# Kernel optimization log

Hardware: AMD Instinct MI355X
Metric: run time of the kernel (lower is better)

Reference implementation:

```python
import jax, jax.numpy as jnp
import numpy as np

# Static config matching init_kwargs
LA = 20.0
GAMMA_INV = 1.0 / 0.1   # self.gamma = 1/gamma
TAU = 0.2
MARGIN = 0.01 * 1.0      # margin * margin_scale
CN = 2
K = 2048
DIM = 128
SUMK = CN * K
B = 16384

# Static intra-class upper-triangular pair mask (same as self.weight in torch)
_blk = np.triu(np.ones((K, K), dtype=bool), k=1)
PAIR_MASK = np.zeros((SUMK, SUMK), dtype=bool)
for _i in range(CN):
    PAIR_MASK[_i * K:(_i + 1) * K, _i * K:(_i + 1) * K] = _blk
PAIR_MASK = jnp.asarray(PAIR_MASK)
N_PAIRS = float(CN * K * (K - 1) // 2)


def setup_inputs() -> dict:
    key = jax.random.key(0)
    k1, k2, k3 = jax.random.split(key, 3)
    x = jax.random.normal(k1, (B, DIM), dtype=jnp.float32)
    target = jax.random.randint(k2, (B,), 0, CN, dtype=jnp.int64)
    fc = jax.random.normal(k3, (DIM, SUMK), dtype=jnp.float32) * 0.05
    return {"x": x, "target": target, "fc": fc}


def reference(x, target, fc):
    # L2-normalize inputs (dim=1) and centers (dim=0)
    norm_input = x / jnp.linalg.norm(x, axis=1, keepdims=True)          # [B, DIM]
    centers = fc / jnp.linalg.norm(fc, axis=0, keepdims=True)           # [DIM, SUMK]

    simInd = norm_input @ centers                                       # [B, SUMK]
    sim = simInd.reshape(B, CN, K)                                      # per-class groups

    # softmax-weighted intra-class similarity (intra_max='softmax')
    prob = jax.nn.softmax(sim * GAMMA_INV, axis=-1)
    simClass = jnp.sum(prob * sim, axis=-1)                             # [B, CN]

    # NOTE: original code sets margin on ALL columns, so uniform shift
    logits = LA * (simClass - MARGIN)

    # cross-entropy, mean reduction (class weights are all 1)
    logp = jax.nn.log_softmax(logits, axis=-1)
    ce = -jnp.take_along_axis(logp, target[:, None].astype(jnp.int32), axis=1).mean()

    # center-pair regularizer (tau > 0, K > 1)
    simCenter = centers.T @ centers                                     # [SUMK, SUMK]
    d = jnp.sqrt(2.0 + 1e-5 - 2.0 * simCenter)                          # >=0 everywhere
    reg = jnp.sum(jnp.where(PAIR_MASK, d, 0.0)) / (N_PAIRS * 2.0)

    loss = ce + TAU * reg
    return loss, logits
```

## Files before the change

### kernel.cpp

```cpp
#include <hip/hip_runtime.h>
#include <math.h>

#define NB 16384
#define DIM 128
#define SUMK 4096
#define KCLS 2048

constexpr float LA = 20.0f;
constexpr float TAU = 0.2f;
constexpr float MARGIN = 0.01f;
constexpr float NPAIRS2 = 8384512.0f;
constexpr float G2L = 14.426950408889634f;
#define CS (8 * NB)

typedef _Float16 half8 __attribute__((ext_vector_type(8)));
typedef float f32x4 __attribute__((ext_vector_type(4)));

#if __has_builtin(__builtin_amdgcn_exp2f)
#define EXP2(v) __builtin_amdgcn_exp2f(v)
#else
#define EXP2(v) exp2f(v)
#endif

#define GLOAD_LDS(SRC, DST)                                                          \
    __builtin_amdgcn_global_load_lds(                                                \
        (const __attribute__((address_space(1))) void*)(SRC),                        \
        (__attribute__((address_space(3))) void*)(DST), 16, 0, 0)

__global__ __launch_bounds__(256) void knorm(const float* __restrict__ fc,
                                             _Float16* __restrict__ cnT) {
    const int t = threadIdx.x;
    const int lane = t & 63;
    const int wid = t >> 6;
    const int c = lane & 15;
    const int q = lane >> 4;
    const int j = blockIdx.x * 64 + wid * 16 + c;

    float v[32];
    const float* p = fc + (size_t)(q * 32) * SUMK + j;
    float ss = 0.f;
#pragma unroll
    for (int i = 0; i < 32; ++i) {
        v[i] = p[(size_t)i * SUMK];
        ss = fmaf(v[i], v[i], ss);
    }
    ss += __shfl_xor(ss, 16);
    ss += __shfl_xor(ss, 32);
    float rn = 1.0f / sqrtf(ss);

    _Float16* w = cnT + (size_t)j * DIM + q * 32;
#pragma unroll
    for (int s = 0; s < 4; ++s) {
        half8 h;
#pragma unroll
        for (int k = 0; k < 8; ++k) h[k] = (_Float16)(v[s * 8 + k] * rn);
        *(half8*)(w + s * 8) = h;
    }
}

__global__ __launch_bounds__(256, 4) void kbig(const float* __restrict__ x,
                                               const _Float16* __restrict__ cnT,
                                               float* __restrict__ pw,
                                               float* __restrict__ reg_acc) {
    __shared__ _Float16 smem[3][2][4][64][8];
    __shared__ float red[4];

    const int t = threadIdx.x;
    const int lane = t & 63;
    const int wid = t >> 6;
    const int m = lane & 15;
    const int kg = lane >> 4;
    const int id = blockIdx.x;

    if (id >= 1024) {
        const int rid = id - 1024;
        const int cls = rid >> 10;
        const int ti = (rid >> 5) & 31;
        const int tj = rid & 31;
        if (tj < ti) return;

        const int i0 = cls * KCLS + ti * 64 + wid * 16;
        const int jb = cls * KCLS + tj * 64;

        const _Float16* aip = cnT + (size_t)(i0 + m) * DIM + kg * 8;
        half8 af[4];
#pragma unroll
        for (int tt = 0; tt < 4; ++tt) af[tt] = *(const half8*)(aip + tt * 32);

        half8 bf[16];
#pragma unroll
        for (int fj = 0; fj < 4; ++fj) {
            const _Float16* bjp = cnT + (size_t)(jb + fj * 16 + m) * DIM + kg * 8;
#pragma unroll
            for (int tt = 0; tt < 4; ++tt) bf[fj * 4 + tt] = *(const half8*)(bjp + tt * 32);
        }

        float local = 0.f;
#pragma unroll
        for (int fj = 0; fj < 4; ++fj) {
            f32x4 cc = {0.f, 0.f, 0.f, 0.f};
#pragma unroll
            for (int tt = 0; tt < 4; ++tt)
                cc = __builtin_amdgcn_mfma_f32_16x16x32_f16(af[tt], bf[fj * 4 + tt], cc, 0, 0, 0);
            int gj = jb + fj * 16 + m;
#pragma unroll
            for (int r = 0; r < 4; ++r) {
                int gi = i0 + kg * 4 + r;
                if (gi < gj)
                    local += sqrtf(fmaxf(2.0f + 1e-5f - 2.f * cc[r], 0.f));
            }
        }
#pragma unroll
        for (int off = 1; off < 64; off <<= 1) local += __shfl_xor(local, off);
        if (lane == 0) red[wid] = local;
        __syncthreads();
        if (t == 0) atomicAdd(reg_acc, (red[0] + red[1]) + (red[2] + red[3]));
        return;
    }

    const int cls = (id >> 7) & 1;
    const int qz = id >> 8;
    const int r0 = (id & 127) * 128 + wid * 32;

    const int q0 = wid * 2, q1 = wid * 2 + 1;
    const int cf0 = q0 >> 2, tt0 = q0 & 3;
    const int cf1 = q1 >> 2, tt1 = q1 & 3;
    const int colbase = cls * KCLS + qz * 512;
    const _Float16* s0 = cnT + (size_t)(colbase + cf0 * 16 + m) * DIM + tt0 * 32 + kg * 8;
    const _Float16* s1 = cnT + (size_t)(colbase + cf1 * 16 + m) * DIM + tt1 * 32 + kg * 8;
    const size_t CSTEP = (size_t)32 * DIM;

#define STAGE(CH, BUF)                                                    \
    do {                                                                  \
        GLOAD_LDS(s0 + (size_t)(CH) * CSTEP, &smem[BUF][cf0][tt0][0][0]); \
        GLOAD_LDS(s1 + (size_t)(CH) * CSTEP, &smem[BUF][cf1][tt1][0][0]); \
    } while (0)

    STAGE(0, 0);
    STAGE(1, 1);

    half8 b0[4], b1[4];
#define LOADX(ROW, BF)                                                        \
    do {                                                                      \
        const float* xp = x + (size_t)(ROW)*DIM + kg * 8;                     \
        float xr[4][8];                                                       \
        float ss = 0.f;                                                       \
        _Pragma("unroll") for (int tt = 0; tt < 4; ++tt) {                    \
            float4 f0 = *(const float4*)(xp + tt * 32);                       \
            float4 f1 = *(const float4*)(xp + tt * 32 + 4);                   \
            xr[tt][0] = f0.x; xr[tt][1] = f0.y; xr[tt][2] = f0.z;             \
            xr[tt][3] = f0.w; xr[tt][4] = f1.x; xr[tt][5] = f1.y;             \
            xr[tt][6] = f1.z; xr[tt][7] = f1.w;                               \
            _Pragma("unroll") for (int qq = 0; qq < 8; ++qq)                  \
                ss = fmaf(xr[tt][qq], xr[tt][qq], ss);                        \
        }                                                                     \
        ss += __shfl_xor(ss, 16);                                             \
        ss += __shfl_xor(ss, 32);                                             \
        float rn = G2L / sqrtf(ss);                                           \
        _Pragma("unroll") for (int tt = 0; tt < 4; ++tt)                      \
            _Pragma("unroll") for (int qq = 0; qq < 8; ++qq)                  \
                BF[tt][qq] = (_Float16)(xr[tt][qq] * rn);                     \
    } while (0)

    LOADX(r0 + m, b0);
    LOADX(r0 + 16 + m, b1);
#undef LOADX

    float rz0 = 0.f, rw0 = 0.f, rz1 = 0.f, rw1 = 0.f;

#define EPI(C, RZ, RW)                                                        \
    do {                                                                      \
        float e0 = EXP2(C[0]);                                                \
        float e1 = EXP2(C[1]);                                                \
        float e2 = EXP2(C[2]);                                                \
        float e3 = EXP2(C[3]);                                                \
        RZ += (e0 + e1) + (e2 + e3);                                          \
        RW += fmaf(e0, C[0], e1 * C[1]) + fmaf(e2, C[2], e3 * C[3]);          \
    } while (0)

    for (int ch = 0; ch < 16; ++ch) {
        __syncthreads();
        if (ch + 2 < 16) STAGE(ch + 2, (ch + 2) % 3);
        const int b = ch % 3;
#pragma unroll
        for (int cf = 0; cf < 2; ++cf) {
            half8 a0 = *(const half8*)&smem[b][cf][0][lane][0];
            half8 a1 = *(const half8*)&smem[b][cf][1][lane][0];
            half8 a2 = *(const half8*)&smem[b][cf][2][lane][0];
            half8 a3 = *(const half8*)&smem[b][cf][3][lane][0];
            f32x4 c0 = {0.f, 0.f, 0.f, 0.f}, c1 = {0.f, 0.f, 0.f, 0.f};
            c0 = __builtin_amdgcn_mfma_f32_16x16x32_f16(a0, b0[0], c0, 0, 0, 0);
            c1 = __builtin_amdgcn_mfma_f32_16x16x32_f16(a0, b1[0], c1, 0, 0, 0);
            c0 = __builtin_amdgcn_mfma_f32_16x16x32_f16(a1, b0[1], c0, 0, 0, 0);
            c1 = __builtin_amdgcn_mfma_f32_16x16x32_f16(a1, b1[1], c1, 0, 0, 0);
            c0 = __builtin_amdgcn_mfma_f32_16x16x32_f16(a2, b0[2], c0, 0, 0, 0);
            c1 = __builtin_amdgcn_mfma_f32_16x16x32_f16(a2, b1[2], c1, 0, 0, 0);
            c0 = __builtin_amdgcn_mfma_f32_16x16x32_f16(a3, b0[3], c0, 0, 0, 0);
            c1 = __builtin_amdgcn_mfma_f32_16x16x32_f16(a3, b1[3], c1, 0, 0, 0);
            EPI(c0, rz0, rw0);
            EPI(c1, rz1, rw1);
        }
    }
#undef EPI
#undef STAGE

    rz0 += __shfl_xor(rz0, 16); rz0 += __shfl_xor(rz0, 32);
    rw0 += __shfl_xor(rw0, 16); rw0 += __shfl_xor(rw0, 32);
    rz1 += __shfl_xor(rz1, 16); rz1 += __shfl_xor(rz1, 32);
    rw1 += __shfl_xor(rw1, 16); rw1 += __shfl_xor(rw1, 32);

    if (lane < 16) {
        const size_t base = (size_t)(cls * 4 + qz) * NB;
        const int rowA = r0 + m, rowB = r0 + 16 + m;
        pw[0 * CS + base + rowA] = rz0;
        pw[0 * CS + base + rowB] = rz1;
        pw[1 * CS + base + rowA] = rw0;
        pw[1 * CS + base + rowB] = rw1;
    }
}

__global__ __launch_bounds__(256) void kce(const float* __restrict__ pw,
                                           const int* __restrict__ tgt,
                                           float* __restrict__ out,
                                           float* __restrict__ ce_acc) {
    int i = blockIdx.x * 256 + threadIdx.x;
    float lg[2];
#pragma unroll
    for (int cls = 0; cls < 2; ++cls) {
        float z = 0.f, w = 0.f;
#pragma unroll
        for (int q = 0; q < 4; ++q) {
            const size_t base = (size_t)(cls * 4 + q) * NB + i;
            z += pw[0 * CS + base];
            w += pw[1 * CS + base];
        }
        lg[cls] = LA * (w / (z * G2L) - MARGIN);
        out[1 + 2 * i + cls] = lg[cls];
    }
    int tg = tgt[i];
    float mx = fmaxf(lg[0], lg[1]);
    float lse = mx + logf(expf(lg[0] - mx) + expf(lg[1] - mx));
    float ce = lse - (tg ? lg[1] : lg[0]);
#pragma unroll
    for (int off = 1; off < 64; off <<= 1) ce += __shfl_xor(ce, off);
    if ((threadIdx.x & 63) == 0) atomicAdd(ce_acc, ce);
}

__global__ void kfin(const float* __restrict__ accum, float* __restrict__ out) {
    out[0] = accum[0] / (float)NB + TAU * (accum[1] / NPAIRS2);
}

extern "C" void kernel_launch(void* const* d_in, const int* in_sizes, int n_in,
                              void* d_out, int out_size, void* d_ws, size_t ws_size,
                              hipStream_t stream) {
    const float* x  = (const float*)d_in[0];
    const int*   tg = (const int*)d_in[1];
    const float* fc = (const float*)d_in[2];
    float* out = (float*)d_out;
    float* ws  = (float*)d_ws;
    float* accum = ws;
    _Float16* cnT = (_Float16*)(ws + 16);
    float* pw = (float*)(cnT + (size_t)SUMK * DIM);

    hipMemsetAsync(accum, 0, 64, stream);
    knorm<<<SUMK / 64, 256, 0, stream>>>(fc, cnT);
    kbig<<<1024 + 2048, 256, 0, stream>>>(x, cnT, pw, accum + 1);
    kce<<<NB / 256, 256, 0, stream>>>(pw, tg, out, accum);
    kfin<<<1, 1, 0, stream>>>(accum, out);
}
```

Baseline: 117.6 us.

## Transpose fc via LDS in knorm, refine kbig staging waits, fold final reduction into kce

knorm now loads fc tiles coalesced into shared memory and transposes them there, replacing the old strided column reads. In kbig, the column-tile staging is issued after the x loads, and the per-chunk __syncthreads is replaced with an explicit vmcnt wait plus s_barrier, with the final chunk peeled out of the loop. kce does a block-level reduction and uses a last-block counter to write the final loss, which removes the separate kfin launch. The explicit vmcnt counts depend on the number of outstanding loads being exactly right, so a miscount could cause a race.

```diff
diff --git a/kernel.cpp b/kernel.cpp
--- a/kernel.cpp
+++ b/kernel.cpp
@@ -29,33 +29,42 @@
 
 __global__ __launch_bounds__(256) void knorm(const float* __restrict__ fc,
                                              _Float16* __restrict__ cnT) {
+    __shared__ float tile[DIM][35];
     const int t = threadIdx.x;
-    const int lane = t & 63;
-    const int wid = t >> 6;
-    const int c = lane & 15;
-    const int q = lane >> 4;
-    const int j = blockIdx.x * 64 + wid * 16 + c;
-
-    float v[32];
-    const float* p = fc + (size_t)(q * 32) * SUMK + j;
+    const int j0 = blockIdx.x * 32;
+
+    const int jr = t & 31;
+    const int dr = t >> 5;
+#pragma unroll
+    for (int it = 0; it < 16; ++it) {
+        int d = it * 8 + dr;
+        tile[d][jr] = fc[(size_t)d * SUMK + j0 + jr];
+    }
+    __syncthreads();
+
+    const int p = t & 7;
+    const int j = t >> 3;
+    float v[16];
     float ss = 0.f;
 #pragma unroll
-    for (int i = 0; i < 32; ++i) {
-        v[i] = p[(size_t)i * SUMK];
+    for (int i = 0; i < 16; ++i) {
+        v[i] = tile[p * 16 + i][j];
         ss = fmaf(v[i], v[i], ss);
     }
-    ss += __shfl_xor(ss, 16);
-    ss += __shfl_xor(ss, 32);
+    ss += __shfl_xor(ss, 1);
+    ss += __shfl_xor(ss, 2);
+    ss += __shfl_xor(ss, 4);
     float rn = 1.0f / sqrtf(ss);
 
-    _Float16* w = cnT + (size_t)j * DIM + q * 32;
-#pragma unroll
-    for (int s = 0; s < 4; ++s) {
-        half8 h;
-#pragma unroll
-        for (int k = 0; k < 8; ++k) h[k] = (_Float16)(v[s * 8 + k] * rn);
-        *(half8*)(w + s * 8) = h;
-    }
+    _Float16* w = cnT + (size_t)(j0 + j) * DIM + p * 16;
+    half8 h0, h1;
+#pragma unroll
+    for (int k = 0; k < 8; ++k) {
+        h0[k] = (_Float16)(v[k] * rn);
+        h1[k] = (_Float16)(v[8 + k] * rn);
+    }
+    *(half8*)w = h0;
+    *(half8*)(w + 8) = h1;
 }
 
 __global__ __launch_bounds__(256, 4) void kbig(const float* __restrict__ x,
@@ -121,23 +130,6 @@
     const int cls = (id >> 7) & 1;
     const int qz = id >> 8;
     const int r0 = (id & 127) * 128 + wid * 32;
-
-    const int q0 = wid * 2, q1 = wid * 2 + 1;
-    const int cf0 = q0 >> 2, tt0 = q0 & 3;
-    const int cf1 = q1 >> 2, tt1 = q1 & 3;
-    const int colbase = cls * KCLS + qz * 512;
-    const _Float16* s0 = cnT + (size_t)(colbase + cf0 * 16 + m) * DIM + tt0 * 32 + kg * 8;
-    const _Float16* s1 = cnT + (size_t)(colbase + cf1 * 16 + m) * DIM + tt1 * 32 + kg * 8;
-    const size_t CSTEP = (size_t)32 * DIM;
-
-#define STAGE(CH, BUF)                                                    \
-    do {                                                                  \
-        GLOAD_LDS(s0 + (size_t)(CH) * CSTEP, &smem[BUF][cf0][tt0][0][0]); \
-        GLOAD_LDS(s1 + (size_t)(CH) * CSTEP, &smem[BUF][cf1][tt1][0][0]); \
-    } while (0)
-
-    STAGE(0, 0);
-    STAGE(1, 1);
 
     half8 b0[4], b1[4];
 #define LOADX(ROW, BF)                                                        \
@@ -166,6 +158,20 @@
     LOADX(r0 + 16 + m, b1);
 #undef LOADX
 
+    const int q0 = wid * 2, q1 = wid * 2 + 1;
+    const int cf0 = q0 >> 2, tt0 = q0 & 3;
+    const int cf1 = q1 >> 2, tt1 = q1 & 3;
+    const int colbase = cls * KCLS + qz * 512;
+    const _Float16* s0 = cnT + (size_t)(colbase + cf0 * 16 + m) * DIM + tt0 * 32 + kg * 8;
+    const _Float16* s1 = cnT + (size_t)(colbase + cf1 * 16 + m) * DIM + tt1 * 32 + kg * 8;
+    const size_t CSTEP = (size_t)32 * DIM;
+
+#define STAGE(CH, BUF)                                                    \
+    do {                                                                  \
+        GLOAD_LDS(s0 + (size_t)(CH) * CSTEP, &smem[BUF][cf0][tt0][0][0]); \
+        GLOAD_LDS(s1 + (size_t)(CH) * CSTEP, &smem[BUF][cf1][tt1][0][0]); \
+    } while (0)
+
     float rz0 = 0.f, rw0 = 0.f, rz1 = 0.f, rw1 = 0.f;
 
 #define EPI(C, RZ, RW)                                                        \
@@ -178,29 +184,40 @@
         RW += fmaf(e0, C[0], e1 * C[1]) + fmaf(e2, C[2], e3 * C[3]);          \
     } while (0)
 
-    for (int ch = 0; ch < 16; ++ch) {
-        __syncthreads();
-        if (ch + 2 < 16) STAGE(ch + 2, (ch + 2) % 3);
-        const int b = ch % 3;
-#pragma unroll
-        for (int cf = 0; cf < 2; ++cf) {
-            half8 a0 = *(const half8*)&smem[b][cf][0][lane][0];
-            half8 a1 = *(const half8*)&smem[b][cf][1][lane][0];
-            half8 a2 = *(const half8*)&smem[b][cf][2][lane][0];
-            half8 a3 = *(const half8*)&smem[b][cf][3][lane][0];
-            f32x4 c0 = {0.f, 0.f, 0.f, 0.f}, c1 = {0.f, 0.f, 0.f, 0.f};
-            c0 = __builtin_amdgcn_mfma_f32_16x16x32_f16(a0, b0[0], c0, 0, 0, 0);
-            c1 = __builtin_amdgcn_mfma_f32_16x16x32_f16(a0, b1[0], c1, 0, 0, 0);
-            c0 = __builtin_amdgcn_mfma_f32_16x16x32_f16(a1, b0[1], c0, 0, 0, 0);
-            c1 = __builtin_amdgcn_mfma_f32_16x16x32_f16(a1, b1[1], c1, 0, 0, 0);
-            c0 = __builtin_amdgcn_mfma_f32_16x16x32_f16(a2, b0[2], c0, 0, 0, 0);
-            c1 = __builtin_amdgcn_mfma_f32_16x16x32_f16(a2, b1[2], c1, 0, 0, 0);
-            c0 = __builtin_amdgcn_mfma_f32_16x16x32_f16(a3, b0[3], c0, 0, 0, 0);
-            c1 = __builtin_amdgcn_mfma_f32_16x16x32_f16(a3, b1[3], c1, 0, 0, 0);
-            EPI(c0, rz0, rw0);
-            EPI(c1, rz1, rw1);
-        }
-    }
+#define COMPUTE(B)                                                            \
+    do {                                                                      \
+        _Pragma("unroll") for (int cf = 0; cf < 2; ++cf) {                    \
+            half8 a0 = *(const half8*)&smem[B][cf][0][lane][0];               \
+            half8 a1 = *(const half8*)&smem[B][cf][1][lane][0];               \
+            half8 a2 = *(const half8*)&smem[B][cf][2][lane][0];               \
+            half8 a3 = *(const half8*)&smem[B][cf][3][lane][0];               \
+            f32x4 c0 = {0.f, 0.f, 0.f, 0.f}, c1 = {0.f, 0.f, 0.f, 0.f};      \
+            c0 = __builtin_amdgcn_mfma_f32_16x16x32_f16(a0, b0[0], c0, 0, 0, 0); \
+            c1 = __builtin_amdgcn_mfma_f32_16x16x32_f16(a0, b1[0], c1, 0, 0, 0); \
+            c0 = __builtin_amdgcn_mfma_f32_16x16x32_f16(a1, b0[1], c0, 0, 0, 0); \
+            c1 = __builtin_amdgcn_mfma_f32_16x16x32_f16(a1, b1[1], c1, 0, 0, 0); \
+            c0 = __builtin_amdgcn_mfma_f32_16x16x32_f16(a2, b0[2], c0, 0, 0, 0); \
+            c1 = __builtin_amdgcn_mfma_f32_16x16x32_f16(a2, b1[2], c1, 0, 0, 0); \
+            c0 = __builtin_amdgcn_mfma_f32_16x16x32_f16(a3, b0[3], c0, 0, 0, 0); \
+            c1 = __builtin_amdgcn_mfma_f32_16x16x32_f16(a3, b1[3], c1, 0, 0, 0); \
+            EPI(c0, rz0, rw0);                                                \
+            EPI(c1, rz1, rw1);                                                \
+        }                                                                     \
+    } while (0)
+
+    STAGE(0, 0);
+    STAGE(1, 1);
+
+    for (int ch = 0; ch < 15; ++ch) {
+        asm volatile("s_waitcnt vmcnt(2)" ::: "memory");
+        __builtin_amdgcn_s_barrier();
+        if (ch < 14) STAGE(ch + 2, (ch + 2) % 3);
+        COMPUTE(ch % 3);
+    }
+    asm volatile("s_waitcnt vmcnt(0)" ::: "memory");
+    __builtin_amdgcn_s_barrier();
+    COMPUTE(0);
+#undef COMPUTE
 #undef EPI
 #undef STAGE
 
@@ -222,8 +239,10 @@
 __global__ __launch_bounds__(256) void kce(const float* __restrict__ pw,
                                            const int* __restrict__ tgt,
                                            float* __restrict__ out,
-                                           float* __restrict__ ce_acc) {
-    int i = blockIdx.x * 256 + threadIdx.x;
+                                           float* __restrict__ accum) {
+    __shared__ float red2[4];
+    const int t = threadIdx.x;
+    int i = blockIdx.x * 256 + t;
     float lg[2];
 #pragma unroll
     for (int cls = 0; cls < 2; ++cls) {
@@ -243,11 +262,18 @@
     float ce = lse - (tg ? lg[1] : lg[0]);
 #pragma unroll
     for (int off = 1; off < 64; off <<= 1) ce += __shfl_xor(ce, off);
-    if ((threadIdx.x & 63) == 0) atomicAdd(ce_acc, ce);
-}
-
-__global__ void kfin(const float* __restrict__ accum, float* __restrict__ out) {
-    out[0] = accum[0] / (float)NB + TAU * (accum[1] / NPAIRS2);
+    if ((t & 63) == 0) red2[t >> 6] = ce;
+    __syncthreads();
+    if (t == 0) {
+        atomicAdd(&accum[0], (red2[0] + red2[1]) + (red2[2] + red2[3]));
+        __threadfence();
+        unsigned old = atomicAdd((unsigned*)&accum[2], 1u);
+        if (old == (unsigned)(NB / 256 - 1)) {
+            float ce_tot = atomicAdd(&accum[0], 0.0f);
+            float reg    = atomicAdd(&accum[1], 0.0f);
+            out[0] = ce_tot / (float)NB + TAU * (reg / NPAIRS2);
+        }
+    }
 }
 
 extern "C" void kernel_launch(void* const* d_in, const int* in_sizes, int n_in,
@@ -263,8 +289,7 @@
     float* pw = (float*)(cnT + (size_t)SUMK * DIM);
 
     hipMemsetAsync(accum, 0, 64, stream);
-    knorm<<<SUMK / 64, 256, 0, stream>>>(fc, cnT);
+    knorm<<<SUMK / 32, 256, 0, stream>>>(fc, cnT);
     kbig<<<1024 + 2048, 256, 0, stream>>>(x, cnT, pw, accum + 1);
     kce<<<NB / 256, 256, 0, stream>>>(pw, tg, out, accum);
-    kfin<<<1, 1, 0, stream>>>(accum, out);
-}
+}
```

Measured after the change: 112.9 us. 1.04x faster.
